# Optimization experiments

Measured on AMD Instinct MI355X. Metric: run time of the kernel, lower is better.

Reference implementation:

```python
import jax, jax.numpy as jnp
import numpy as np

# Default DigitCaps config: reduced_votes=False, iter=1, softmax=False, tanh_like=False,
# l_thetas=[1.0], lr_som=1.0, radical=False, no normalization, no winner-ratio bookkeeping.
H, Wd, INPUT_F, INPUT_D = 12, 12, 32, 8
C, D, M = 10, 8, 4          # num_out_caps, vector_depth, transf_mat_for_each_caps
LR, THETA = 1.0, 1.0


def setup_inputs() -> dict:
    key = jax.random.key(0)
    k1, k2, k3 = jax.random.split(key, 3)
    B = 128
    inputs = jax.random.normal(k1, (B, H, Wd, INPUT_F, INPUT_D), dtype=jnp.float32)
    J = H * Wd * INPUT_F  # 4608 positions
    # he_normal over fan_in = INPUT_D
    W = jax.random.normal(k2, (J, INPUT_D, D * M), dtype=jnp.float32) * jnp.sqrt(2.0 / INPUT_D)
    digit_caps = jax.random.uniform(k3, (C, D), minval=-1.0, maxval=1.0, dtype=jnp.float32)
    return {"inputs": inputs, "W": W, "digit_caps": digit_caps}


def reference(inputs, W, digit_caps):
    B = inputs.shape[0]
    J = H * Wd * INPUT_F
    x = inputs.reshape(B, J, INPUT_D)
    # per-position transform: [B,J,input_d] x [J,input_d,D*M] -> [B,J,D*M]
    u = jnp.einsum('bji,jik->bjk', x, W)
    N = J * M
    u = u.reshape(B, N, D)  # votes (broadcast over C instead of tiling)

    # similarities[b,n,c] = <u[b,n], digit_caps[c]>
    sims = jnp.einsum('bnd,cd->bnc', u, digit_caps)
    winners = jnp.argmax(sims, axis=-1)  # [B, N] int

    # sparse_updates = one_hot(winners) * (u - digit_caps) * lr * theta;
    # updates = mean over (B, N). Computed via segment-sum (honors winner sparsity).
    flat_w = winners.reshape(-1)
    flat_u = u.reshape(-1, D)
    seg_u = jax.ops.segment_sum(flat_u, flat_w, num_segments=C)          # [C, D]
    counts = jnp.zeros((C,), jnp.float32).at[flat_w].add(1.0)            # [C]
    denom = jnp.float32(B * N)
    updates = (seg_u - counts[:, None] * digit_caps) * (LR * THETA) / denom

    digit_caps_new = digit_caps + updates  # assign_add happens before final sims

    sims_final = jnp.einsum('bnd,cd->bnc', u, digit_caps_new)
    output = jnp.mean(sims_final, axis=-2)  # [B, C]
    return output, digit_caps_new
```

## Files before the change

kernel.cpp:

```cpp
#include <hip/hip_runtime.h>


#define J_POS 4608
#define SEGSTRIDE 97
#define NSEG 32
#define SSTRIDE 520
#define NSREP 8
#define NVOTES 18432.0f
#define DENOM  2359296.0f
#define SEG_SCALE 32768.0f
#define INV_SEG_SCALE 3.0517578125e-5f
#define OFF_PART_SEG 64
#define OFF_PART_S   110656
#define OFF_S_FINAL  700480
#define OFF_SEG_PART_LL 350752

__global__ __launch_bounds__(256, 4) void votes_kernel(
    const float* __restrict__ x,
    const float* __restrict__ w,
    const float* __restrict__ dc,
    int* __restrict__ part_seg,
    int* __restrict__ part_s,
    int* __restrict__ done)
{
    __shared__ int seg_lds[NSEG * SEGSTRIDE];
    __shared__ int s_lds[NSREP * SSTRIDE];

    const int t  = threadIdx.x;
    const int jg = blockIdx.x >> 1;
    const int h  = blockIdx.x & 1;
    const int j0 = jg * 8;

    if (blockIdx.x == 0 && t == 0) *done = 0;

    for (int i = t; i < NSEG * SEGSTRIDE; i += 256) seg_lds[i] = 0;
    for (int i = t; i < NSREP * SSTRIDE; i += 256) s_lds[i] = 0;

    const int jj   = t >> 5;
    const int m    = (t >> 3) & 3;
    const int brow = t & 7;
    const int j = j0 + jj;

    float4 wra[8], wrb[8];
    {
        const float* wp = w + (size_t)j * 256 + m * 8;
        #pragma unroll
        for (int i = 0; i < 8; ++i) {
            wra[i] = *(const float4*)(wp + i * 32);
            wrb[i] = *(const float4*)(wp + i * 32 + 4);
        }
    }

    float dcs[80];
    #pragma unroll
    for (int c = 0; c < 10; ++c) {
        const float4 a = *(const float4*)(dc + c * 8);
        const float4 b = *(const float4*)(dc + c * 8 + 4);
        dcs[c*8+0] = __uint_as_float(__builtin_amdgcn_readfirstlane(__float_as_uint(a.x)));
        dcs[c*8+1] = __uint_as_float(__builtin_amdgcn_readfirstlane(__float_as_uint(a.y)));
        dcs[c*8+2] = __uint_as_float(__builtin_amdgcn_readfirstlane(__float_as_uint(a.z)));
        dcs[c*8+3] = __uint_as_float(__builtin_amdgcn_readfirstlane(__float_as_uint(a.w)));
        dcs[c*8+4] = __uint_as_float(__builtin_amdgcn_readfirstlane(__float_as_uint(b.x)));
        dcs[c*8+5] = __uint_as_float(__builtin_amdgcn_readfirstlane(__float_as_uint(b.y)));
        dcs[c*8+6] = __uint_as_float(__builtin_amdgcn_readfirstlane(__float_as_uint(b.z)));
        dcs[c*8+7] = __uint_as_float(__builtin_amdgcn_readfirstlane(__float_as_uint(b.w)));
    }

    int* const segp = &seg_lds[((t >> 1) & (NSEG - 1)) * SEGSTRIDE];
    int* const sp = &s_lds[((t >> 3) & (NSREP - 1)) * SSTRIDE];

    __syncthreads();

    const float* xp0 = x + ((size_t)(h * 64 + brow) * J_POS + j) * 8;
    float4 nx0 = *(const float4*)xp0;
    float4 nx1 = *(const float4*)(xp0 + 4);

    #pragma unroll 1
    for (int it = 0; it < 8; ++it) {
        const int bl = it * 8 + brow;
        const float4 x0 = nx0, x1 = nx1;
        if (it < 7) {
            const float* xp = x + ((size_t)(h * 64 + bl + 8) * J_POS + j) * 8;
            nx0 = *(const float4*)xp;
            nx1 = *(const float4*)(xp + 4);
        }
        const float xf[8] = {x0.x,x0.y,x0.z,x0.w,x1.x,x1.y,x1.z,x1.w};

        float u[8] = {0,0,0,0,0,0,0,0};
        #pragma unroll
        for (int i = 0; i < 8; ++i) {
            const float xi = xf[i];
            u[0] += xi * wra[i].x; u[1] += xi * wra[i].y;
            u[2] += xi * wra[i].z; u[3] += xi * wra[i].w;
            u[4] += xi * wrb[i].x; u[5] += xi * wrb[i].y;
            u[6] += xi * wrb[i].z; u[7] += xi * wrb[i].w;
        }

        float best = -3.402823466e38f;
        int bc = 0;
        #pragma unroll
        for (int c = 0; c < 10; ++c) {
            const float sim = u[0]*dcs[c*8+0] + u[1]*dcs[c*8+1]
                            + u[2]*dcs[c*8+2] + u[3]*dcs[c*8+3]
                            + u[4]*dcs[c*8+4] + u[5]*dcs[c*8+5]
                            + u[6]*dcs[c*8+6] + u[7]*dcs[c*8+7];
            if (sim > best) { best = sim; bc = c; }
        }

        const int o = bc * 9;
        const int sb = bl * 8;
        #pragma unroll
        for (int d = 0; d < 8; ++d) {
            const int q = __float2int_rn(u[d] * SEG_SCALE);
            atomicAdd(&segp[o + d], q);
            atomicAdd(&sp[sb + d], q);
        }
        atomicAdd(&segp[o + 8], 1);
    }

    __syncthreads();

    if (t < 90) {
        int v = 0;
        #pragma unroll
        for (int r = 0; r < NSEG; ++r) v += seg_lds[r * SEGSTRIDE + t];
        part_seg[blockIdx.x * 96 + t] = v;
    }
    #pragma unroll
    for (int e = t; e < 512; e += 256) {
        int v = 0;
        #pragma unroll
        for (int r = 0; r < NSREP; ++r) v += s_lds[r * SSTRIDE + e];
        part_s[(size_t)blockIdx.x * 512 + e] = v;
    }
}

__global__ __launch_bounds__(256) void reduce_final_kernel(
    const int* __restrict__ part_seg,
    const int* __restrict__ part_s,
    float* __restrict__ s_final,
    long long* __restrict__ seg_part,
    int* __restrict__ done,
    const float* __restrict__ dc,
    float* __restrict__ out)
{
    __shared__ long long red[64][5];
    __shared__ long long segred[2][96];
    __shared__ float dcn[80];
    __shared__ float sf[1024];
    __shared__ int lastflag;

    const int t = threadIdx.x;
    const int bid = blockIdx.x;

    if (bid < 16) {
        const int g0 = bid * 64;
        const int h = g0 >> 9;
        const int gl = t & 63, chunk = t >> 6;
        const int col = (g0 + gl) & 511;
        long long acc = 0;
        #pragma unroll 8
        for (int i = chunk * 144; i < chunk * 144 + 144; ++i)
            acc += part_s[(size_t)(2 * i + h) * 512 + col];
        red[gl][chunk] = acc;
        __syncthreads();
        if (t < 64) {
            const long long v = red[t][0] + red[t][1] + red[t][2] + red[t][3];
            __hip_atomic_store(&s_final[g0 + t], (float)v * INV_SEG_SCALE,
                               __ATOMIC_RELAXED, __HIP_MEMORY_SCOPE_AGENT);
        }
    } else {
        const int p = bid - 16;
        if (t < 192) {
            const int o = t % 96, rc = t / 96;
            long long acc = 0;
            const int r0 = p * 288 + rc * 144;
            #pragma unroll 8
            for (int i = r0; i < r0 + 144; ++i)
                acc += part_seg[(size_t)i * 96 + o];
            segred[rc][o] = acc;
        }
        __syncthreads();
        if (t < 96)
            __hip_atomic_store(&seg_part[p * 96 + t], segred[0][t] + segred[1][t],
                               __ATOMIC_RELAXED, __HIP_MEMORY_SCOPE_AGENT);
    }

    __threadfence();
    __syncthreads();
    if (t == 0) lastflag = (atomicAdd(done, 1) == 19) ? 1 : 0;
    __syncthreads();
    if (!lastflag) return;
    __threadfence();

    #pragma unroll
    for (int r = 0; r < 4; ++r) {
        const int i = r * 256 + t;
        const float v = __hip_atomic_load(&s_final[i], __ATOMIC_RELAXED,
                                          __HIP_MEMORY_SCOPE_AGENT);
        sf[i] = v * (1.0f / NVOTES);
    }
    if (t < 80) {
        const int c = t >> 3, d = t & 7;
        long long sv = 0, cv = 0;
        #pragma unroll
        for (int p = 0; p < 4; ++p) {
            sv += __hip_atomic_load(&seg_part[p * 96 + c * 9 + d], __ATOMIC_RELAXED,
                                    __HIP_MEMORY_SCOPE_AGENT);
            cv += __hip_atomic_load(&seg_part[p * 96 + c * 9 + 8], __ATOMIC_RELAXED,
                                    __HIP_MEMORY_SCOPE_AGENT);
        }
        const float d0 = dc[t];
        const float nd = d0 + ((float)sv * INV_SEG_SCALE - (float)cv * d0) * (1.0f / DENOM);
        dcn[t] = nd;
        out[1280 + t] = nd;
    }
    __syncthreads();

    #pragma unroll
    for (int r = 0; r < 5; ++r) {
        const int idx = r * 256 + t;
        const int b = idx / 10, c = idx - b * 10;
        float acc = 0.f;
        #pragma unroll
        for (int d = 0; d < 8; ++d) acc += sf[b * 8 + d] * dcn[c * 8 + d];
        out[idx] = acc;
    }
}

extern "C" void kernel_launch(void* const* d_in, const int* in_sizes, int n_in,
                              void* d_out, int out_size, void* d_ws, size_t ws_size,
                              hipStream_t stream) {
    const float* x  = (const float*)d_in[0];
    const float* w  = (const float*)d_in[1];
    const float* dc = (const float*)d_in[2];
    float* out = (float*)d_out;
    int*       done      = (int*)d_ws;
    int*       part_seg  = (int*)d_ws + OFF_PART_SEG;
    int*       part_s    = (int*)d_ws + OFF_PART_S;
    float*     s_final   = (float*)d_ws + OFF_S_FINAL;
    long long* seg_part  = (long long*)d_ws + OFF_SEG_PART_LL;

    votes_kernel<<<1152, 256, 0, stream>>>(x, w, dc, part_seg, part_s, done);
    reduce_final_kernel<<<20, 256, 0, stream>>>(part_seg, part_s, s_final,
                                                seg_part, done, dc, out);
}
```

Before: 100.2 us.

## Fuse the reduction into the votes kernel with global atomics and a last-block finalize

Result: slower. 170.8 us (+70.5%).

```diff
diff --git a/kernel.cpp b/kernel.cpp
--- a/kernel.cpp
+++ b/kernel.cpp
@@ -10,28 +10,26 @@
 #define DENOM  2359296.0f
 #define SEG_SCALE 32768.0f
 #define INV_SEG_SCALE 3.0517578125e-5f
-#define OFF_PART_SEG 64
-#define OFF_PART_S   110656
-#define OFF_S_FINAL  700480
-#define OFF_SEG_PART_LL 350752
 
 __global__ __launch_bounds__(256, 4) void votes_kernel(
     const float* __restrict__ x,
     const float* __restrict__ w,
     const float* __restrict__ dc,
-    int* __restrict__ part_seg,
-    int* __restrict__ part_s,
-    int* __restrict__ done)
+    long long* __restrict__ g_seg,
+    int* __restrict__ g_s,
+    int* __restrict__ done,
+    float* __restrict__ out)
 {
     __shared__ int seg_lds[NSEG * SEGSTRIDE];
     __shared__ int s_lds[NSREP * SSTRIDE];
+    __shared__ float sf[1024];
+    __shared__ float dcn[80];
+    __shared__ int lastflag;
 
     const int t  = threadIdx.x;
     const int jg = blockIdx.x >> 1;
     const int h  = blockIdx.x & 1;
     const int j0 = jg * 8;
-
-    if (blockIdx.x == 0 && t == 0) *done = 0;
 
     for (int i = t; i < NSEG * SEGSTRIDE; i += 256) seg_lds[i] = 0;
     for (int i = t; i < NSREP * SSTRIDE; i += 256) s_lds[i] = 0;
@@ -124,71 +122,20 @@
         int v = 0;
         #pragma unroll
         for (int r = 0; r < NSEG; ++r) v += seg_lds[r * SEGSTRIDE + t];
-        part_seg[blockIdx.x * 96 + t] = v;
+        atomicAdd((unsigned long long*)&g_seg[t],
+                  (unsigned long long)(long long)v);
     }
     #pragma unroll
     for (int e = t; e < 512; e += 256) {
         int v = 0;
         #pragma unroll
         for (int r = 0; r < NSREP; ++r) v += s_lds[r * SSTRIDE + e];
-        part_s[(size_t)blockIdx.x * 512 + e] = v;
-    }
-}
-
-__global__ __launch_bounds__(256) void reduce_final_kernel(
-    const int* __restrict__ part_seg,
-    const int* __restrict__ part_s,
-    float* __restrict__ s_final,
-    long long* __restrict__ seg_part,
-    int* __restrict__ done,
-    const float* __restrict__ dc,
-    float* __restrict__ out)
-{
-    __shared__ long long red[64][5];
-    __shared__ long long segred[2][96];
-    __shared__ float dcn[80];
-    __shared__ float sf[1024];
-    __shared__ int lastflag;
-
-    const int t = threadIdx.x;
-    const int bid = blockIdx.x;
-
-    if (bid < 16) {
-        const int g0 = bid * 64;
-        const int h = g0 >> 9;
-        const int gl = t & 63, chunk = t >> 6;
-        const int col = (g0 + gl) & 511;
-        long long acc = 0;
-        #pragma unroll 8
-        for (int i = chunk * 144; i < chunk * 144 + 144; ++i)
-            acc += part_s[(size_t)(2 * i + h) * 512 + col];
-        red[gl][chunk] = acc;
-        __syncthreads();
-        if (t < 64) {
-            const long long v = red[t][0] + red[t][1] + red[t][2] + red[t][3];
-            __hip_atomic_store(&s_final[g0 + t], (float)v * INV_SEG_SCALE,
-                               __ATOMIC_RELAXED, __HIP_MEMORY_SCOPE_AGENT);
-        }
-    } else {
-        const int p = bid - 16;
-        if (t < 192) {
-            const int o = t % 96, rc = t / 96;
-            long long acc = 0;
-            const int r0 = p * 288 + rc * 144;
-            #pragma unroll 8
-            for (int i = r0; i < r0 + 144; ++i)
-                acc += part_seg[(size_t)i * 96 + o];
-            segred[rc][o] = acc;
-        }
-        __syncthreads();
-        if (t < 96)
-            __hip_atomic_store(&seg_part[p * 96 + t], segred[0][t] + segred[1][t],
-                               __ATOMIC_RELAXED, __HIP_MEMORY_SCOPE_AGENT);
+        atomicAdd(&g_s[h * 512 + e], v);
     }
 
     __threadfence();
     __syncthreads();
-    if (t == 0) lastflag = (atomicAdd(done, 1) == 19) ? 1 : 0;
+    if (t == 0) lastflag = (atomicAdd(done, 1) == 1151) ? 1 : 0;
     __syncthreads();
     if (!lastflag) return;
     __threadfence();
@@ -196,20 +143,16 @@
     #pragma unroll
     for (int r = 0; r < 4; ++r) {
         const int i = r * 256 + t;
-        const float v = __hip_atomic_load(&s_final[i], __ATOMIC_RELAXED,
-                                          __HIP_MEMORY_SCOPE_AGENT);
-        sf[i] = v * (1.0f / NVOTES);
+        const int v = __hip_atomic_load(&g_s[i], __ATOMIC_RELAXED,
+                                        __HIP_MEMORY_SCOPE_AGENT);
+        sf[i] = (float)v * INV_SEG_SCALE * (1.0f / NVOTES);
     }
     if (t < 80) {
         const int c = t >> 3, d = t & 7;
-        long long sv = 0, cv = 0;
-        #pragma unroll
-        for (int p = 0; p < 4; ++p) {
-            sv += __hip_atomic_load(&seg_part[p * 96 + c * 9 + d], __ATOMIC_RELAXED,
-                                    __HIP_MEMORY_SCOPE_AGENT);
-            cv += __hip_atomic_load(&seg_part[p * 96 + c * 9 + 8], __ATOMIC_RELAXED,
-                                    __HIP_MEMORY_SCOPE_AGENT);
-        }
+        const long long sv = __hip_atomic_load(&g_seg[c * 9 + d], __ATOMIC_RELAXED,
+                                               __HIP_MEMORY_SCOPE_AGENT);
+        const long long cv = __hip_atomic_load(&g_seg[c * 9 + 8], __ATOMIC_RELAXED,
+                                               __HIP_MEMORY_SCOPE_AGENT);
         const float d0 = dc[t];
         const float nd = d0 + ((float)sv * INV_SEG_SCALE - (float)cv * d0) * (1.0f / DENOM);
         dcn[t] = nd;
@@ -235,13 +178,10 @@
     const float* w  = (const float*)d_in[1];
     const float* dc = (const float*)d_in[2];
     float* out = (float*)d_out;
-    int*       done      = (int*)d_ws;
-    int*       part_seg  = (int*)d_ws + OFF_PART_SEG;
-    int*       part_s    = (int*)d_ws + OFF_PART_S;
-    float*     s_final   = (float*)d_ws + OFF_S_FINAL;
-    long long* seg_part  = (long long*)d_ws + OFF_SEG_PART_LL;
+    int*       done  = (int*)d_ws;
+    long long* g_seg = (long long*)((char*)d_ws + 64);
+    int*       g_s   = (int*)((char*)d_ws + 1024);
 
-    votes_kernel<<<1152, 256, 0, stream>>>(x, w, dc, part_seg, part_s, done);
-    reduce_final_kernel<<<20, 256, 0, stream>>>(part_seg, part_s, s_final,
-                                                seg_part, done, dc, out);
+    hipMemsetAsync(d_ws, 0, 5120, stream);
+    votes_kernel<<<1152, 256, 0, stream>>>(x, w, dc, g_seg, g_s, done, out);
 }
```
